# Kernel tuning notes

Hardware: AMD Instinct MI355X
Metric: run time of the kernel (lower is better)

Reference implementation:

```python
import jax, jax.numpy as jnp
from jax import lax
import numpy as np

EPS = 1e-5
DN = ('NCHW', 'OIHW', 'NCHW')


def conv_s2(x, w):
    # Conv2d k=4 s=2 p=1, no bias
    return lax.conv_general_dilated(x, w, (2, 2), [(1, 1), (1, 1)], dimension_numbers=DN)


def deconv_s2(x, w):
    # ConvTranspose2d k=4 s=2 p=1; torch weight layout (in, out, kH, kW)
    w_ = jnp.flip(w, (2, 3)).transpose(1, 0, 2, 3)  # -> (out, in, kH, kW)
    return lax.conv_general_dilated(x, w_, (1, 1), [(2, 2), (2, 2)],
                                    lhs_dilation=(2, 2), dimension_numbers=DN)


def bn_train(x, gamma, beta):
    # BatchNorm2d in training mode: batch stats over (N, H, W), biased variance
    m = jnp.mean(x, axis=(0, 2, 3), keepdims=True)
    v = jnp.var(x, axis=(0, 2, 3), keepdims=True)
    g = gamma.reshape(1, -1, 1, 1)
    b = beta.reshape(1, -1, 1, 1)
    return (x - m) * jax.lax.rsqrt(v + EPS) * g + b


def lrelu(x):
    return jnp.where(x >= 0, x, 0.2 * x)


def setup_inputs() -> dict:
    key = jax.random.key(0)
    ks = jax.random.split(key, 32)
    nef = 64
    d = {}
    d['x'] = jax.random.normal(ks[0], (256, 3, 64, 64), dtype=jnp.float32)
    # encoder conv weights (O, I, 4, 4), init N(0, 0.02)
    d['w1'] = 0.02 * jax.random.normal(ks[1], (nef, 3, 4, 4), jnp.float32)
    d['w2'] = 0.02 * jax.random.normal(ks[2], (nef * 2, nef, 4, 4), jnp.float32)
    d['w3'] = 0.02 * jax.random.normal(ks[3], (nef * 4, nef * 2, 4, 4), jnp.float32)
    d['w4'] = 0.02 * jax.random.normal(ks[4], (nef * 8, nef * 4, 4, 4), jnp.float32)
    # bn params: weight ~ N(1, 0.02), bias = 0
    for i, c in enumerate([nef, nef * 2, nef * 4, nef * 8]):
        d[f'g{i+1}'] = 1.0 + 0.02 * jax.random.normal(ks[5 + i], (c,), jnp.float32)
        d[f'b{i+1}'] = jnp.zeros((c,), jnp.float32)
    # 512 channel-wise Linear(16,16): torch default init U(-1/4, 1/4)
    bound = 1.0 / 4.0
    d['cw_w'] = jax.random.uniform(ks[9], (512, 16, 16), jnp.float32, -bound, bound)
    d['cw_b'] = jax.random.uniform(ks[10], (512, 16), jnp.float32, -bound, bound)
    # decoder deconv weights in torch layout (in, out, 4, 4)
    d['dw1'] = 0.02 * jax.random.normal(ks[11], (nef * 8, nef * 4, 4, 4), jnp.float32)
    d['dw2'] = 0.02 * jax.random.normal(ks[12], (nef * 4, nef * 2, 4, 4), jnp.float32)
    d['dw3'] = 0.02 * jax.random.normal(ks[13], (nef * 2, nef, 4, 4), jnp.float32)
    d['dw4'] = 0.02 * jax.random.normal(ks[14], (nef, 3, 4, 4), jnp.float32)
    for i, c in enumerate([nef * 4, nef * 2, nef]):
        d[f'dg{i+1}'] = 1.0 + 0.02 * jax.random.normal(ks[15 + i], (c,), jnp.float32)
        d[f'db{i+1}'] = jnp.zeros((c,), jnp.float32)
    return d


def reference(x, w1, w2, w3, w4, g1, b1, g2, b2, g3, b3, g4, b4,
              cw_w, cw_b, dw1, dw2, dw3, dw4, dg1, db1, dg2, db2, dg3, db3):
    h = lrelu(bn_train(conv_s2(x, w1), g1, b1))
    h = lrelu(bn_train(conv_s2(h, w2), g2, b2))
    h = lrelu(bn_train(conv_s2(h, w3), g3, b3))
    h = lrelu(bn_train(conv_s2(h, w4), g4, b4))  # (B, 512, 4, 4)
    B, C, H, W = h.shape
    flat = h.reshape(B, C, H * W)  # (B, 512, 16)
    # per-channel Linear: y[b,c,t] = sum_s flat[b,c,s] * cw_w[c,t,s] + cw_b[c,t]
    flat = jnp.einsum('bcs,cts->bct', flat, cw_w) + cw_b[None, :, :]
    h = flat.reshape(B, C, H, W)
    h = jax.nn.relu(bn_train(deconv_s2(h, dw1), dg1, db1))
    h = jax.nn.relu(bn_train(deconv_s2(h, dw2), dg2, db2))
    h = jax.nn.relu(bn_train(deconv_s2(h, dw3), dg3, db3))
    return jnp.tanh(deconv_s2(h, dw4))
```

## Files before the change

kernel.cpp:

```cpp
#include <hip/hip_runtime.h>
#include <math.h>

typedef _Float16 f16;
typedef __attribute__((ext_vector_type(8))) _Float16 f16x8;
typedef __attribute__((ext_vector_type(16))) float f32x16;

union U64x2 { unsigned long long u[2]; f16x8 v; };
union Q16   { uint4 q; unsigned long long u[2]; };

constexpr int ilog2c(int x) { return x <= 1 ? 0 : 1 + ilog2c(x >> 1); }

__device__ __forceinline__ float fast_tanh(float x) {
    float e = __expf(2.f * x);
    return (e - 1.f) / (e + 1.f);
}

__device__ __forceinline__ void barrier_no_vmdrain() {
    asm volatile("s_waitcnt lgkmcnt(0)" ::: "memory");
    __builtin_amdgcn_sched_barrier(0);
    __builtin_amdgcn_s_barrier();
    __builtin_amdgcn_sched_barrier(0);
}

template<int CIN,int IH,int IW,int OH,int OW,int COUT,int COB,int SPT,int KS,
         int CO_FR,bool DEC,bool PAIR>
__global__ __launch_bounds__(256,2) void mfma_conv(
    const f16* __restrict__ xin, const f16* __restrict__ wp,
    f16* __restrict__ out16, float* __restrict__ out32, size_t ps,
    float* __restrict__ psumF, float* __restrict__ psqF)
{
    constexpr int OHo  = DEC ? OH/2 : OH;
    constexpr int OWo  = DEC ? OW/2 : OW;
    constexpr int KTOT = CIN * (DEC ? 4 : 16);
    constexpr int CH   = (KTOT/64) / KS;
    constexpr int RPT  = CIN / 64;
    constexpr int RSH  = (RPT==1?0:RPT==2?1:RPT==4?2:3);
    constexpr int WSTR = CIN * 16;
    constexpr int TPR  = 256 / COB;
    constexpr int SPB  = OHo * OWo;
    constexpr int LSPB = ilog2c(SPB);
    constexpr int LOWo = ilog2c(OWo);

    static_assert(!PAIR || (RPT >= 2 && CH % 2 == 0), "PAIR needs RPT>=2");
    constexpr int CHU  = PAIR ? CH/2 : CH;
    constexpr int RW   = PAIR ? 32 : 16;
    constexpr int PM   = PAIR ? 15 : 7;
    constexpr int KKN  = PAIR ? 8 : 4;
    constexpr int XU4  = PAIR ? 16 : 8;
    constexpr int WSEG = (PAIR ? 128 : 64)/TPR;
    constexpr int WU4  = WSEG / 8;

    __shared__ unsigned long long Xs[SPT*RW];
    __shared__ unsigned long long Wls[COB*RW];

    const int t   = threadIdx.x;
    const int bx  = blockIdx.x;
    const int cob = blockIdx.y;
    const int bz  = blockIdx.z;
    const int par = DEC ? (bz & 3) : 0;
    const int ks  = DEC ? (bz >> 2) : bz;
    const int poh = par >> 1, pw = par & 1;

    const int gsp_s = bx*SPT + t;
    const int img_s = gsp_s >> LSPB;
    const int r_s   = gsp_s & (SPB-1);
    const int oy_s  = r_s >> LOWo;
    const int ox_s  = r_s & (OWo-1);

    const int wco   = t / TPR;
    const int wpart = t % TPR;
    const f16* wbase = wp + (size_t)(cob*COB + wco)*WSTR + wpart*WSEG;

    const int wave = t >> 6, lane = t & 63, half = lane >> 5, l31 = lane & 31;
    const int co_w = (wave >> 1) * (CO_FR*32);
    const int sp_w = (wave & 1) * 128;
    const int swz  = l31 & PM;

    f32x16 acc[CO_FR][4];
    #pragma unroll
    for (int i = 0; i < CO_FR; ++i)
        #pragma unroll
        for (int b = 0; b < 4; ++b)
            #pragma unroll
            for (int r = 0; r < 16; ++r) acc[i][b][r] = 0.f;

    uint4 xreg[XU4];
    uint4 wreg[WU4];

    auto issue = [&](int cc) {
        const int gc  = ks*CH + (PAIR ? 2*cc : cc);
        const int tap = gc >> RSH;
        const int ci0 = (gc & (RPT-1)) << 6;
        int kh, kw, ih, iw;
        if (DEC) {
            const int t2h = tap >> 1, t2w = tap & 1;
            kh = (1-poh) + 2*t2h; kw = (1-pw) + 2*t2w;
            ih = oy_s + poh - t2h; iw = ox_s + pw - t2w;
        } else {
            kh = tap >> 2; kw = tap & 3;
            ih = 2*oy_s - 1 + kh; iw = 2*ox_s - 1 + kw;
        }
        const int woff = (kh*4 + kw)*CIN + ci0;
        const uint4* wsrc = (const uint4*)(wbase + woff);
        #pragma unroll
        for (int j = 0; j < WU4; ++j) wreg[j] = wsrc[j];
        const bool ok = (unsigned)ih < (unsigned)IH && (unsigned)iw < (unsigned)IW;
        if (ok) {
            const uint4* xsrc = (const uint4*)
                (xin + ((size_t)(img_s*IH + ih)*IW + iw)*CIN + ci0);
            #pragma unroll
            for (int j = 0; j < XU4; ++j) xreg[j] = xsrc[j];
        } else {
            #pragma unroll
            for (int j = 0; j < XU4; ++j) xreg[j] = uint4{0u,0u,0u,0u};
        }
    };

    issue(0);

    for (int cc = 0; cc < CHU; ++cc) {
        if (cc) barrier_no_vmdrain();

        #pragma unroll
        for (int j = 0; j < WU4; ++j) {
            Q16 v; v.q = wreg[j];
            const int lp = wpart*WU4 + j;
            const int u0 = wco*RW + ((lp ^ (wco & PM)) << 1);
            Wls[u0]   = v.u[0];
            Wls[u0+1] = v.u[1];
        }
        {
            #pragma unroll
            for (int j = 0; j < XU4; ++j) {
                Q16 v; v.q = xreg[j];
                const int u0 = t*RW + ((j ^ (t & PM)) << 1);
                Xs[u0]   = v.u[0];
                Xs[u0+1] = v.u[1];
            }
        }

        if (cc + 1 < CHU) issue(cc + 1);

        asm volatile("s_waitcnt lgkmcnt(0)" ::: "memory");
        __builtin_amdgcn_sched_barrier(0);
        __builtin_amdgcn_s_barrier();
        __builtin_amdgcn_sched_barrier(0);

        #pragma unroll
        for (int kk = 0; kk < KKN; ++kk) {
            const int so = ((kk*2 + half) ^ swz) << 1;
            f16x8 wf[CO_FR], xf[4];
            #pragma unroll
            for (int i = 0; i < CO_FR; ++i) {
                U64x2 u; const int rw = (co_w + i*32 + l31)*RW + so;
                u.u[0] = Wls[rw]; u.u[1] = Wls[rw+1]; wf[i] = u.v;
            }
            #pragma unroll
            for (int b = 0; b < 4; ++b) {
                U64x2 u; const int rx = (sp_w + b*32 + l31)*RW + so;
                u.u[0] = Xs[rx]; u.u[1] = Xs[rx+1]; xf[b] = u.v;
            }
            #pragma unroll
            for (int i = 0; i < CO_FR; ++i)
                #pragma unroll
                for (int b = 0; b < 4; ++b)
                    acc[i][b] = __builtin_amdgcn_mfma_f32_32x32x16_f16(
                        xf[b], wf[i], acc[i][b], 0, 0, 0);
        }
    }

    #pragma unroll
    for (int b = 0; b < 4; ++b) {
        #pragma unroll
        for (int q = 0; q < 4; ++q) {
            #pragma unroll
            for (int r2 = 0; r2 < 4; ++r2) {
                const int sp_loc = sp_w + b*32 + q*8 + 4*half + r2;
                const int gsp    = bx*SPT + sp_loc;
                size_t base;
                if (DEC) {
                    const int img = gsp >> LSPB;
                    const int r   = gsp & (SPB-1);
                    const int oh  = 2*(r >> LOWo) + poh;
                    const int ow  = 2*(r & (OWo-1)) + pw;
                    base = ((size_t)(img*OH + oh)*OW + ow)*COUT + cob*COB;
                } else {
                    base = (size_t)gsp*COUT + cob*COB;
                }
                #pragma unroll
                for (int i = 0; i < CO_FR; ++i) {
                    const int co_l = co_w + i*32 + l31;
                    const float v  = acc[i][b][q*4 + r2];
                    if (KS == 1) out16[base + co_l] = (_Float16)v;
                    else         out32[(size_t)ks*ps + base + co_l] = v;
                }
            }
        }
    }

    if (KS == 1 && psumF != nullptr) {
        float sArr[CO_FR], qArr[CO_FR];
        #pragma unroll
        for (int i = 0; i < CO_FR; ++i) {
            float s = 0.f, q = 0.f;
            #pragma unroll
            for (int b = 0; b < 4; ++b)
                #pragma unroll
                for (int r = 0; r < 16; ++r) {
                    const float v = acc[i][b][r];
                    s += v; q += v * v;
                }
            s += __shfl_down(s, 32);
            q += __shfl_down(q, 32);
            sArr[i] = s; qArr[i] = q;
        }
        __syncthreads();
        float* LS = (float*)Xs;
        float* LQ = LS + 4*CO_FR*32;
        if (half == 0) {
            #pragma unroll
            for (int i = 0; i < CO_FR; ++i) {
                LS[(wave*CO_FR + i)*32 + l31] = sArr[i];
                LQ[(wave*CO_FR + i)*32 + l31] = qArr[i];
            }
        }
        __syncthreads();
        if (t < COB) {
            constexpr int KSH = (CO_FR == 1 ? 5 : 6);
            const int k  = t >> KSH;
            const int ii = (CO_FR == 1) ? 0 : ((t >> 5) & 1);
            const int l  = t & 31;
            const int i0 = ((2*k)  *CO_FR + ii)*32 + l;
            const int i1 = ((2*k+1)*CO_FR + ii)*32 + l;
            atomicAdd(psumF + cob*COB + t, LS[i0] + LS[i1]);
            atomicAdd(psqF  + cob*COB + t, LQ[i0] + LQ[i1]);
        }
    }
}

__global__ __launch_bounds__(256,2) void conv1_mfma(
    const f16* __restrict__ xp, const f16* __restrict__ wp,
    f16* __restrict__ out, float* __restrict__ psumF, float* __restrict__ psqF)
{
    __shared__ unsigned long long Xs[256*16];
    __shared__ unsigned long long Wls[64*16];
    const int t = threadIdx.x, bx = blockIdx.x;

    {
        const int r = t >> 2, part = t & 3;
        const uint4* src = (const uint4*)(wp + r*64 + part*16);
        Q16 v0; v0.q = src[0];
        Q16 v1; v1.q = src[1];
        const int a0 = r*16 + (((part*2)   ^ (r & 7)) << 1);
        const int a1 = r*16 + (((part*2+1) ^ (r & 7)) << 1);
        Wls[a0]   = v0.u[0]; Wls[a0+1] = v0.u[1];
        Wls[a1]   = v1.u[0]; Wls[a1+1] = v1.u[1];
    }
    {
        const int gsp = bx*256 + t;
        const int n = gsp >> 10, r = gsp & 1023;
        const int oy = r >> 5, ox = r & 31;
        const int ih0 = 2*oy - 1, iw0 = 2*ox - 1;
        #pragma unroll
        for (int tap = 0; tap < 16; ++tap) {
            const int ih = ih0 + (tap >> 2), iw = iw0 + (tap & 3);
            unsigned long long v = 0ull;
            if ((unsigned)ih < 64u && (unsigned)iw < 64u)
                v = *(const unsigned long long*)(xp + (((size_t)n*64 + ih)*64 + iw)*4);
            const int u = t*16 + (((tap >> 1) ^ (t & 7)) << 1) + (tap & 1);
            Xs[u] = v;
        }
    }
    __syncthreads();

    const int wave = t >> 6, lane = t & 63, half = lane >> 5, l31 = lane & 31;
    const int co_w = (wave >> 1) * 32;
    const int sp_w = (wave & 1) * 128;
    const int swz  = l31 & 7;

    f32x16 acc[4];
    #pragma unroll
    for (int b = 0; b < 4; ++b)
        #pragma unroll
        for (int r = 0; r < 16; ++r) acc[b][r] = 0.f;

    #pragma unroll
    for (int kk = 0; kk < 4; ++kk) {
        const int so = ((kk*2 + half) ^ swz) << 1;
        U64x2 uw; const int rw = (co_w + l31)*16 + so;
        uw.u[0] = Wls[rw]; uw.u[1] = Wls[rw+1];
        #pragma unroll
        for (int b = 0; b < 4; ++b) {
            U64x2 ux; const int rx = (sp_w + b*32 + l31)*16 + so;
            ux.u[0] = Xs[rx]; ux.u[1] = Xs[rx+1];
            acc[b] = __builtin_amdgcn_mfma_f32_32x32x16_f16(
                ux.v, uw.v, acc[b], 0, 0, 0);
        }
    }
    #pragma unroll
    for (int b = 0; b < 4; ++b)
        #pragma unroll
        for (int q = 0; q < 4; ++q)
            #pragma unroll
            for (int r2 = 0; r2 < 4; ++r2) {
                const int sp_loc = sp_w + b*32 + q*8 + 4*half + r2;
                out[(size_t)(bx*256 + sp_loc)*64 + co_w + l31] =
                    (_Float16)acc[b][q*4 + r2];
            }

    float s = 0.f, q = 0.f;
    #pragma unroll
    for (int b = 0; b < 4; ++b)
        #pragma unroll
        for (int r = 0; r < 16; ++r) {
            const float v = acc[b][r];
            s += v; q += v * v;
        }
    s += __shfl_down(s, 32);
    q += __shfl_down(q, 32);
    __syncthreads();
    {
        float* LS = (float*)Xs;
        float* LQ = LS + 128;
        if (half == 0) {
            LS[wave*32 + l31] = s;
            LQ[wave*32 + l31] = q;
        }
        __syncthreads();
        if (t < 64) {
            const int k = t >> 5, l = t & 31;
            atomicAdd(psumF + t, LS[(2*k)*32 + l] + LS[(2*k+1)*32 + l]);
            atomicAdd(psqF  + t, LQ[(2*k)*32 + l] + LQ[(2*k+1)*32 + l]);
        }
    }
}

__global__ __launch_bounds__(256,2) void deconv3_pwf(
    const f16* __restrict__ xin, const f16* __restrict__ wp,
    f16* __restrict__ out, float* __restrict__ psumF, float* __restrict__ psqF)
{
    __shared__ unsigned long long Xs[256*16];
    __shared__ unsigned long long Wls[2][64*16];

    const int t   = threadIdx.x;
    const int bx  = blockIdx.x;
    const int poh = blockIdx.y;

    const int gsp_s = bx*256 + t;
    const int img_s = gsp_s >> 8;
    const int r_s   = gsp_s & 255;
    const int oy_s  = r_s >> 4;
    const int ox_s  = r_s & 15;

    const int wco   = t >> 2;
    const int wpart = t & 3;
    const f16* wbase = wp + (size_t)wco*2048 + wpart*16;

    const int wave = t >> 6, lane = t & 63, half = lane >> 5, l31 = lane & 31;
    const int co_w = (wave >> 1) * 32;
    const int sp_w = (wave & 1) * 128;
    const int swz  = l31 & 7;

    f32x16 acc[2][4];
    #pragma unroll
    for (int p = 0; p < 2; ++p)
        #pragma unroll
        for (int b = 0; b < 4; ++b)
            #pragma unroll
            for (int r = 0; r < 16; ++r) acc[p][b][r] = 0.f;

    uint4 xreg[8];
    uint4 wregP[2][2];

    auto issue = [&](int cc) {
        const int seg  = cc & 1;
        const int rest = cc >> 1;
        const int dwi  = rest % 3;
        const int t2h  = rest / 3;
        const int dh = poh - t2h, dw = dwi - 1;
        const int ih = oy_s + dh, iw = ox_s + dw;
        const int ci0 = seg << 6;
        #pragma unroll
        for (int p = 0; p < 2; ++p) {
            const int t2w = p - dw;
            if (t2w == 0 || t2w == 1) {
                const int kh = (1-poh) + 2*t2h, kw = (1-p) + 2*t2w;
                const uint4* wsrc = (const uint4*)(wbase + (kh*4 + kw)*128 + ci0);
                wregP[p][0] = wsrc[0];
                wregP[p][1] = wsrc[1];
            }
        }
        const bool ok = (unsigned)ih < 16u && (unsigned)iw < 16u;
        if (ok) {
            const uint4* xsrc = (const uint4*)
                (xin + ((size_t)(img_s*16 + ih)*16 + iw)*128 + ci0);
            #pragma unroll
            for (int j = 0; j < 8; ++j) xreg[j] = xsrc[j];
        } else {
            #pragma unroll
            for (int j = 0; j < 8; ++j) xreg[j] = uint4{0u,0u,0u,0u};
        }
    };

    issue(0);

    for (int cc = 0; cc < 12; ++cc) {
        const int rest = cc >> 1;
        const int dw   = rest % 3 - 1;

        if (cc) barrier_no_vmdrain();

        #pragma unroll
        for (int p = 0; p < 2; ++p) {
            const int t2w = p - dw;
            if (t2w == 0 || t2w == 1) {
                #pragma unroll
                for (int j = 0; j < 2; ++j) {
                    Q16 v; v.q = wregP[p][j];
                    const int lp = wpart*2 + j;
                    const int u0 = wco*16 + ((lp ^ (wco & 7)) << 1);
                    Wls[p][u0]   = v.u[0];
                    Wls[p][u0+1] = v.u[1];
                }
            }
        }
        #pragma unroll
        for (int j = 0; j < 8; ++j) {
            Q16 v; v.q = xreg[j];
            const int u0 = t*16 + ((j ^ (t & 7)) << 1);
            Xs[u0]   = v.u[0];
            Xs[u0+1] = v.u[1];
        }

        if (cc + 1 < 12) issue(cc + 1);

        asm volatile("s_waitcnt lgkmcnt(0)" ::: "memory");
        __builtin_amdgcn_sched_barrier(0);
        __builtin_amdgcn_s_barrier();
        __builtin_amdgcn_sched_barrier(0);

        #pragma unroll
        for (int kk = 0; kk < 4; ++kk) {
            const int so = ((kk*2 + half) ^ swz) << 1;
            f16x8 xf[4];
            #pragma unroll
            for (int b = 0; b < 4; ++b) {
                U64x2 u; const int rx = (sp_w + b*32 + l31)*16 + so;
                u.u[0] = Xs[rx]; u.u[1] = Xs[rx+1]; xf[b] = u.v;
            }
            #pragma unroll
            for (int p = 0; p < 2; ++p) {
                const int t2w = p - dw;
                if (t2w == 0 || t2w == 1) {
                    U64x2 uw; const int rw = (co_w + l31)*16 + so;
                    uw.u[0] = Wls[p][rw]; uw.u[1] = Wls[p][rw+1];
                    #pragma unroll
                    for (int b = 0; b < 4; ++b)
                        acc[p][b] = __builtin_amdgcn_mfma_f32_32x32x16_f16(
                            xf[b], uw.v, acc[p][b], 0, 0, 0);
                }
            }
        }
    }

    #pragma unroll
    for (int p = 0; p < 2; ++p) {
        #pragma unroll
        for (int b = 0; b < 4; ++b) {
            #pragma unroll
            for (int q = 0; q < 4; ++q) {
                #pragma unroll
                for (int r2 = 0; r2 < 4; ++r2) {
                    const int sp_loc = sp_w + b*32 + q*8 + 4*half + r2;
                    const int gsp    = bx*256 + sp_loc;
                    const int img    = gsp >> 8;
                    const int r      = gsp & 255;
                    const int oh     = 2*(r >> 4) + poh;
                    const int ow     = 2*(r & 15) + p;
                    const size_t base = ((size_t)(img*32 + oh)*32 + ow)*64;
                    out[base + co_w + l31] = (_Float16)acc[p][b][q*4 + r2];
                }
            }
        }
    }

    if (psumF != nullptr) {
        float s = 0.f, q = 0.f;
        #pragma unroll
        for (int p = 0; p < 2; ++p)
            #pragma unroll
            for (int b = 0; b < 4; ++b)
                #pragma unroll
                for (int r = 0; r < 16; ++r) {
                    const float v = acc[p][b][r];
                    s += v; q += v * v;
                }
        s += __shfl_down(s, 32);
        q += __shfl_down(q, 32);
        __syncthreads();
        float* LS = (float*)Xs;
        float* LQ = LS + 128;
        if (half == 0) {
            LS[wave*32 + l31] = s;
            LQ[wave*32 + l31] = q;
        }
        __syncthreads();
        if (t < 64) {
            const int k = t >> 5, l = t & 31;
            atomicAdd(psumF + t, LS[(2*k)*32 + l] + LS[(2*k+1)*32 + l]);
            atomicAdd(psqF  + t, LQ[(2*k)*32 + l] + LQ[(2*k+1)*32 + l]);
        }
    }
}

static constexpr int D4P0[4] = {0,0,1,1};
static constexpr int D4KH0[4]= {3,3,3,3};
static constexpr int D4KW0[4]= {3,1,2,0};
static constexpr int D4DW0[4]= {-1,0,0,1};
static constexpr int D4P1[8] = {0,0,1,1,2,2,3,3};
static constexpr int D4KH1[8]= {1,1,1,1,2,2,2,2};
static constexpr int D4KW1[8]= {3,1,2,0,3,1,2,0};
static constexpr int D4DW1[8]= {-1,0,0,1,-1,0,0,1};
static constexpr int D4P2[4] = {2,2,3,3};
static constexpr int D4KH2[4]= {0,0,0,0};
static constexpr int D4KW2[4]= {3,1,2,0};
static constexpr int D4DW2[4]= {-1,0,0,1};

#define D4_PHASE(DH, PA, KHA, KWA, DWA, NC, LEAD, HASNEXT, NEXTDH)           \
    {                                                                        \
        if (LEAD) barrier_no_vmdrain();                                      \
        uint4 wregc[NC];                                                     \
        _Pragma("unroll")                                                    \
        for (int i = 0; i < NC; ++i)                                         \
            wregc[i] = *(const uint4*)                                       \
                (wp + wco*1024 + (KHA[i]*4 + KWA[i])*64 + wpart*8);          \
        {                                                                    \
            const int c7 = colA & 7;                                         \
            _Pragma("unroll")                                                \
            for (int j = 0; j < 8; ++j) {                                    \
                Q16 v; v.q = xreg[j];                                        \
                const int u0 = t*16 + ((j ^ c7) << 1);                       \
                Xs[u0] = v.u[0]; Xs[u0+1] = v.u[1];                          \
            }                                                                \
        }                                                                    \
        if ((t & 15) == 0) {                                                 \
            const int u2 = 256 + (t >> 4);                                   \
            const int col2 = u2 - 238;               \
            const int iy = R0 + (DH) + 7, ix = col2 - 1;                     \
            const int c7 = col2 & 7;                                         \
            const bool ok = (unsigned)iy < 32u && (unsigned)ix < 32u;        \
            if (ok) {                                                        \
                const uint4* s = (const uint4*)                              \
                    (xin + ((size_t)(img*32 + iy)*32 + ix)*64);              \
                _Pragma("unroll")                                            \
                for (int j = 0; j < 8; ++j) {                                \
                    Q16 v; v.q = s[j];                                       \
                    const int u0 = u2*16 + ((j ^ c7) << 1);                  \
                    Xs[u0] = v.u[0]; Xs[u0+1] = v.u[1];                      \
                }                                                            \
            } else {                                                         \
                _Pragma("unroll")                                            \
                for (int j = 0; j < 8; ++j) {                                \
                    const int u0 = u2*16 + ((j ^ c7) << 1);                  \
                    Xs[u0] = 0ull; Xs[u0+1] = 0ull;                          \
                }                                                            \
            }                                                                \
        }                                                                    \
        _Pragma("unroll")                                                    \
        for (int i = 0; i < NC; ++i) {                                       \
            Q16 v; v.q = wregc[i];                                           \
            const int u0 = wco*16 + ((wpart ^ (wco & 7)) << 1);              \
            Wls[i][u0] = v.u[0]; Wls[i][u0+1] = v.u[1];                      \
        }                                                                    \
        if (HASNEXT) issueX(NEXTDH);                                         \
        asm volatile("s_waitcnt lgkmcnt(0)" ::: "memory");                   \
        __builtin_amdgcn_sched_barrier(0);                                   \
        __builtin_amdgcn_s_barrier();                                        \
        __builtin_amdgcn_sched_barrier(0);                                   \
        _Pragma("unroll")                                                    \
        for (int i = 0; i < NC; ++i) {                                       \
            const int dwv = DWA[i], p = PA[i];                               \
            const int colx = l31 + dwv + 1;                                  \
            const int cx7  = colx & 7;                                       \
            _Pragma("unroll")                                                \
            for (int kk = 0; kk < 4; ++kk) {                                 \
                const int sw = ((kk*2 + half) ^ (l31 & 7)) << 1;             \
                const int sx = ((kk*2 + half) ^ cx7) << 1;                   \
                U64x2 uw; const int rwi = l31*16 + sw;                       \
                uw.u[0] = Wls[i][rwi]; uw.u[1] = Wls[i][rwi+1];              \
                _Pragma("unroll")                                            \
                for (int b = 0; b < 2; ++b) {                                \
                    const int unit = (wave*2 + b)*34 + colx;                 \
                    U64x2 ux; const int rx = unit*16 + sx;                   \
                    ux.u[0] = Xs[rx]; ux.u[1] = Xs[rx+1];                    \
                    acc[p][b] = __builtin_amdgcn_mfma_f32_32x32x16_f16(      \
                        uw.v, ux.v, acc[p][b], 0, 0, 0);                     \
                }                                                            \
            }                                                                \
        }                                                                    \
    }

__global__ __launch_bounds__(256,2) void deconv4_mfma(
    const f16* __restrict__ xin, const f16* __restrict__ wp,
    float* __restrict__ out)
{
    __shared__ unsigned long long Xs[272*16];
    __shared__ unsigned long long Wls[8][32*16];

    const int t   = threadIdx.x;
    const int bx  = blockIdx.x;

    const int img = (bx*256) >> 10;
    const int R0  = ((bx*256) & 1023) >> 5;

    const int wco   = t >> 3;
    const int wpart = t & 7;

    const int wave = t >> 6, lane = t & 63, half = lane >> 5, l31 = lane & 31;
    const int sp_w = wave * 64;

    const int rowA = t / 34, colA = t % 34;

    f32x16 acc[4][2];
    #pragma unroll
    for (int p = 0; p < 4; ++p)
        #pragma unroll
        for (int b = 0; b < 2; ++b)
            #pragma unroll
            for (int r = 0; r < 16; ++r) acc[p][b][r] = 0.f;

    uint4 xreg[8];

    auto issueX = [&](int dh) {
        const int iy = R0 + dh + rowA, ix = colA - 1;
        const bool ok = (unsigned)iy < 32u && (unsigned)ix < 32u;
        if (ok) {
            const uint4* s = (const uint4*)
                (xin + ((size_t)(img*32 + iy)*32 + ix)*64);
            #pragma unroll
            for (int j = 0; j < 8; ++j) xreg[j] = s[j];
        } else {
            #pragma unroll
            for (int j = 0; j < 8; ++j) xreg[j] = uint4{0u,0u,0u,0u};
        }
    };

    issueX(-1);

    D4_PHASE(-1, D4P0, D4KH0, D4KW0, D4DW0, 4, false, true, 0)
    D4_PHASE( 0, D4P1, D4KH1, D4KW1, D4DW1, 8, true,  true, 1)
    D4_PHASE( 1, D4P2, D4KH2, D4KW2, D4DW2, 4, true,  false, 0)

    if (half == 0) {
        #pragma unroll
        for (int p = 0; p < 4; ++p) {
            const int poh = p >> 1, pw = p & 1;
            #pragma unroll
            for (int b = 0; b < 2; ++b) {
                const int gsp = bx*256 + sp_w + b*32 + l31;
                const int im  = gsp >> 10;
                const int r   = gsp & 1023;
                const int oh  = 2*(r >> 5) + poh;
                const int ow  = 2*(r & 31) + pw;
                #pragma unroll
                for (int co = 0; co < 3; ++co)
                    out[(((size_t)im*3 + co)*64 + oh)*64 + ow] =
                        fast_tanh(acc[p][b][co]);
            }
        }
    }
}

__global__ __launch_bounds__(256) void prep_x(
    const float* __restrict__ x, f16* __restrict__ xp)
{
    const int i = blockIdx.x*256 + threadIdx.x;
    const int n = i >> 12, p = i & 4095;
    const float* b = x + (size_t)n*12288 + p;
    union { _Float16 h[4]; unsigned long long u; } o;
    o.h[0] = (_Float16)b[0];
    o.h[1] = (_Float16)b[4096];
    o.h[2] = (_Float16)b[8192];
    o.h[3] = (_Float16)0.f;
    *(unsigned long long*)(xp + (size_t)i*4) = o.u;
}

__global__ __launch_bounds__(256) void prep_w1(
    const float* __restrict__ w1, f16* __restrict__ wp)
{
    const int e = blockIdx.x*256 + threadIdx.x;
    const int co = e >> 6, k = e & 63, tap = k >> 2, ci = k & 3;
    const float v = (ci < 3) ? w1[(co*3 + ci)*16 + tap] : 0.f;
    wp[e] = (_Float16)v;
}

__global__ __launch_bounds__(256) void prep_w4(
    const float* __restrict__ dw4, f16* __restrict__ wp)
{
    const int e = blockIdx.x*256 + threadIdx.x;
    const int co = e >> 10, r = e & 1023, khw = r >> 6, ci = r & 63;
    const float v = (co < 3) ? dw4[(ci*3 + co)*16 + khw] : 0.f;
    wp[e] = (_Float16)v;
}

__global__ __launch_bounds__(256) void prep_w(
    const float* __restrict__ w2, const float* __restrict__ w3,
    const float* __restrict__ w4, const float* __restrict__ dw1,
    const float* __restrict__ dw2, const float* __restrict__ dw3,
    f16* __restrict__ dst)
{
    const int e = blockIdx.x*256 + threadIdx.x;
    float v;
    if (e < 131072) {
        int co = e >> 10, r = e & 1023, khw = r >> 6, ci = r & 63;
        v = w2[(co*64 + ci)*16 + khw];
    } else if (e < 655360) {
        int l = e - 131072;
        int co = l >> 11, r = l & 2047, khw = r >> 7, ci = r & 127;
        v = w3[(co*128 + ci)*16 + khw];
    } else if (e < 2752512) {
        int l = e - 655360;
        int co = l >> 12, r = l & 4095, khw = r >> 8, ci = r & 255;
        v = w4[(co*256 + ci)*16 + khw];
    } else if (e < 4849664) {
        int l = e - 2752512;
        int co = l >> 13, r = l & 8191, khw = r >> 9, ci = r & 511;
        v = dw1[(ci*256 + co)*16 + khw];
    } else if (e < 5373952) {
        int l = e - 4849664;
        int co = l >> 12, r = l & 4095, khw = r >> 8, ci = r & 255;
        v = dw2[(ci*128 + co)*16 + khw];
    } else {
        int l = e - 5373952;
        int co = l >> 11, r = l & 2047, khw = r >> 7, ci = r & 127;
        v = dw3[(ci*64 + co)*16 + khw];
    }
    dst[e] = (_Float16)v;
}

template<typename T, int P>
__global__ __launch_bounds__(256) void bn_partial(
    const T* __restrict__ x, size_t ps, float* __restrict__ psum,
    float* __restrict__ psq, int C, int rowsPerS, int S)
{
    const int s = blockIdx.x;
    const int c = (blockIdx.y << 6) + (threadIdx.x & 63);
    float a = 0.f, q = 0.f;
    const int rEnd = (s + 1) * rowsPerS;
    for (int r = s*rowsPerS + (threadIdx.x >> 6); r < rEnd; r += 4) {
        float v = 0.f;
        #pragma unroll
        for (int p = 0; p < P; ++p)
            v += (float)x[p*ps + (size_t)r * C + c];
        a += v; q += v * v;
    }
    __shared__ float ls[256], lq[256];
    ls[threadIdx.x] = a; lq[threadIdx.x] = q;
    __syncthreads();
    if (threadIdx.x < 64) {
        a = ls[threadIdx.x] + ls[threadIdx.x+64] + ls[threadIdx.x+128] + ls[threadIdx.x+192];
        q = lq[threadIdx.x] + lq[threadIdx.x+64] + lq[threadIdx.x+128] + lq[threadIdx.x+192];
        psum[c * S + s] = a; psq[c * S + s] = q;
    }
}

__global__ __launch_bounds__(256) void bn_finalize(
    const float* __restrict__ psum, const float* __restrict__ psq,
    const float* __restrict__ gamma, const float* __restrict__ beta,
    float* __restrict__ scale, float* __restrict__ shift,
    int C, int S, float inv_count)
{
    int c = blockIdx.x * 256 + threadIdx.x;
    if (c >= C) return;
    float s = 0.f, q = 0.f;
    for (int i = 0; i < S; ++i) { s += psum[c*S + i]; q += psq[c*S + i]; }
    float m   = s * inv_count;
    float var = q * inv_count - m * m;
    var = var < 0.f ? 0.f : var;
    float sc = gamma[c] * rsqrtf(var + 1e-5f);
    scale[c] = sc;
    shift[c] = beta[c] - m * sc;
}

__global__ __launch_bounds__(256) void bn_act16f(
    f16* __restrict__ x, const float* __restrict__ psum, const float* __restrict__ psq,
    const float* __restrict__ gamma, const float* __restrict__ beta,
    int Cmask, float inv_count, float slope, size_t n8)
{
    const size_t base = (size_t)blockIdx.x*256 + threadIdx.x;
    const int c0 = (int)((base * 8) & (size_t)Cmask);
    float sc[8], sh[8];
    #pragma unroll
    for (int j = 0; j < 8; ++j) {
        const int c = c0 + j;
        float m   = psum[c] * inv_count;
        float var = psq[c] * inv_count - m * m;
        var = var < 0.f ? 0.f : var;
        float s = gamma[c] * rsqrtf(var + 1e-5f);
        sc[j] = s;
        sh[j] = beta[c] - m * s;
    }
    const size_t stride = (size_t)gridDim.x * 256;
    for (size_t i = base; i < n8; i += stride) {
        union { uint4 u; _Float16 h[8]; } a;
        a.u = *(const uint4*)(x + i*8);
        #pragma unroll
        for (int j = 0; j < 8; ++j) {
            float v = (float)a.h[j] * sc[j] + sh[j];
            a.h[j] = (_Float16)(v >= 0.f ? v : slope * v);
        }
        *(uint4*)(x + i*8) = a.u;
    }
}

template<int P>
__global__ __launch_bounds__(256) void bn_act32(
    const float* __restrict__ x, size_t ps, f16* __restrict__ y,
    const float* __restrict__ sc, const float* __restrict__ sh,
    int Cmask, float slope)
{
    const size_t i8 = ((size_t)blockIdx.x*256 + threadIdx.x) * 8;
    float xv[8] = {0,0,0,0,0,0,0,0};
    #pragma unroll
    for (int p = 0; p < P; ++p) {
        float4 v0 = *(const float4*)(x + p*ps + i8);
        float4 v1 = *(const float4*)(x + p*ps + i8 + 4);
        xv[0]+=v0.x; xv[1]+=v0.y; xv[2]+=v0.z; xv[3]+=v0.w;
        xv[4]+=v1.x; xv[5]+=v1.y; xv[6]+=v1.z; xv[7]+=v1.w;
    }
    union { uint4 u; _Float16 h[8]; } a;
    const int c0 = (int)(i8 & (size_t)Cmask);
    #pragma unroll
    for (int j = 0; j < 8; ++j) {
        float v = xv[j] * sc[c0+j] + sh[c0+j];
        a.h[j] = (_Float16)(v >= 0.f ? v : slope * v);
    }
    *(uint4*)(y + i8) = a.u;
}

__global__ __launch_bounds__(256) void chanlin16(
    const f16* __restrict__ in, const float* __restrict__ w,
    const float* __restrict__ bias, f16* __restrict__ out)
{
    const int i = blockIdx.x*256 + threadIdx.x;
    const int c  = i & 511;
    const int bt = i >> 9;
    const int b  = bt >> 4, tt = bt & 15;
    const f16* src = in + ((size_t)b*16)*512 + c;
    const float* wr = w + ((size_t)c*16 + tt)*16;
    float acc = bias[c*16 + tt];
    #pragma unroll
    for (int s = 0; s < 16; ++s)
        acc = fmaf((float)src[s*512], wr[s], acc);
    out[i] = (_Float16)acc;
}

extern "C" void kernel_launch(void* const* d_in, const int* in_sizes, int n_in,
                              void* d_out, int out_size, void* d_ws, size_t ws_size,
                              hipStream_t stream)
{
    const float* x   = (const float*)d_in[0];
    const float* w1  = (const float*)d_in[1];
    const float* w2  = (const float*)d_in[2];
    const float* w3  = (const float*)d_in[3];
    const float* w4  = (const float*)d_in[4];
    const float* g1  = (const float*)d_in[5];
    const float* b1  = (const float*)d_in[6];
    const float* g2  = (const float*)d_in[7];
    const float* b2  = (const float*)d_in[8];
    const float* g3  = (const float*)d_in[9];
    const float* b3  = (const float*)d_in[10];
    const float* g4  = (const float*)d_in[11];
    const float* b4  = (const float*)d_in[12];
    const float* cww = (const float*)d_in[13];
    const float* cwb = (const float*)d_in[14];
    const float* dw1 = (const float*)d_in[15];
    const float* dw2 = (const float*)d_in[16];
    const float* dw3 = (const float*)d_in[17];
    const float* dw4 = (const float*)d_in[18];
    const float* dg1 = (const float*)d_in[19];
    const float* db1 = (const float*)d_in[20];
    const float* dg2 = (const float*)d_in[21];
    const float* db2 = (const float*)d_in[22];
    const float* dg3 = (const float*)d_in[23];
    const float* db3 = (const float*)d_in[24];

    char* WS = (char*)d_ws;
    float* psum  = (float*)WS;
    float* psq   = (float*)(WS + 65536);
    float* scale = (float*)(WS + 131072);
    float* shift = (float*)(WS + 133120);
    float* fst   = (float*)(WS + 196608);
    f16* slotA   = (f16*)(WS + 262144);
    f16* slotB   = (f16*)(WS + 262144 + 33554432);
    f16* wprep   = (f16*)(WS + 84148224);
    f16* wprep1  = wprep + 5505024;
    f16* wprep4  = wprep1 + 4096;

    f16*   A_hi  = slotA + 8388608;
    float* pB    = (float*)slotB;
    f16*   xpack = slotA;

    float* fs0 = fst;          float* fs1 = fst + 1024;
    float* fs2 = fst + 2048;   float* fs4 = fst + 4096;
    float* fs5 = fst + 5120;   float* fs6 = fst + 6144;

    hipMemsetAsync(fst, 0, 28672, stream);
    prep_w<<<21504, 256, 0, stream>>>(w2, w3, w4, dw1, dw2, dw3, wprep);
    prep_w1<<<16, 256, 0, stream>>>(w1, wprep1);
    prep_w4<<<128, 256, 0, stream>>>(dw4, wprep4);
    prep_x<<<4096, 256, 0, stream>>>(x, xpack);

    conv1_mfma<<<1024, 256, 0, stream>>>(xpack, wprep1, slotB, fs0, fs0 + 512);
    bn_act16f<<<2048, 256, 0, stream>>>(slotB, fs0, fs0 + 512, g1, b1, 63,
                                        1.f/262144.f, 0.2f, (size_t)2097152);

    mfma_conv<64,32,32,16,16,128, 128,256,1,2,false,false><<<dim3(256,1,1), 256, 0, stream>>>(
        slotB, wprep, slotA, nullptr, 0, fs1, fs1 + 512);
    bn_act16f<<<2048, 256, 0, stream>>>(slotA, fs1, fs1 + 512, g2, b2, 127,
                                        1.f/65536.f, 0.2f, (size_t)1048576);

    mfma_conv<128,16,16,8,8,256, 64,256,1,1,false,false><<<dim3(64,4,1), 256, 0, stream>>>(
        slotA, wprep + 131072, A_hi, nullptr, 0, fs2, fs2 + 512);
    bn_act16f<<<2048, 256, 0, stream>>>(A_hi, fs2, fs2 + 512, g3, b3, 255,
                                        1.f/16384.f, 0.2f, (size_t)524288);

    mfma_conv<256,8,8,4,4,512, 128,256,4,2,false,false><<<dim3(16,4,4), 256, 0, stream>>>(
        A_hi, wprep + 655360, nullptr, pB, (size_t)2097152, nullptr, nullptr);
    bn_partial<float,4><<<dim3(32,8), 256, 0, stream>>>(pB, (size_t)2097152, psum, psq, 512, 128, 32);
    bn_finalize<<<2, 256, 0, stream>>>(psum, psq, g4, b4, scale, shift, 512, 32, 1.f/4096.f);
    bn_act32<4><<<1024, 256, 0, stream>>>(pB, (size_t)2097152, slotA, scale, shift, 511, 0.2f);

    chanlin16<<<8192, 256, 0, stream>>>(slotA, cww, cwb, slotB);

    mfma_conv<512,4,4,8,8,256, 64,256,1,1,true,false><<<dim3(16,4,4), 256, 0, stream>>>(
        slotB, wprep + 2752512, A_hi, nullptr, 0, fs4, fs4 + 512);
    bn_act16f<<<2048, 256, 0, stream>>>(A_hi, fs4, fs4 + 512, dg1, db1, 255,
                                        1.f/16384.f, 0.f, (size_t)524288);

    mfma_conv<256,8,8,16,16,128, 128,256,1,2,true,false><<<dim3(64,1,4), 256, 0, stream>>>(
        A_hi, wprep + 4849664, slotB, nullptr, 0, fs5, fs5 + 512);
    bn_act16f<<<2048, 256, 0, stream>>>(slotB, fs5, fs5 + 512, dg2, db2, 127,
                                        1.f/65536.f, 0.f, (size_t)1048576);

    deconv3_pwf<<<dim3(256,2), 256, 0, stream>>>(
        slotB, wprep + 5373952, slotA, fs6, fs6 + 512);
    bn_act16f<<<2048, 256, 0, stream>>>(slotA, fs6, fs6 + 512, dg3, db3, 63,
                                        1.f/262144.f, 0.f, (size_t)2097152);

    deconv4_mfma<<<1024, 256, 0, stream>>>(slotA, wprep4, (float*)d_out);
}
```

Baseline: 520.5 us.

## Stage halo-padded input tile once per row phase and reuse across column taps

The deconv3 kernel now processes one image per block and loads a 16x18 column-halo-padded input tile into shared memory. MFMA reads then index shifted columns for each of the four (p, dw) taps, instead of reloading the input from global memory for every dw offset. This cuts the main loop from 12 chunks to 4 phases and reduces global input traffic. The cost is more shared memory for the tile and four weight slices, an extra partial load for halo rows, and more irregular swizzled LDS addressing.

```diff
diff --git a/kernel.cpp b/kernel.cpp
--- a/kernel.cpp
+++ b/kernel.cpp
@@ -335,22 +335,25 @@
     }
 }
 
+static constexpr int D3P[4]  = {0, 0, 1, 1};
+static constexpr int D3DW[4] = {0,-1, 1, 0};
+static constexpr int D3KW[4] = {1, 3, 0, 2};
+
 __global__ __launch_bounds__(256,2) void deconv3_pwf(
     const f16* __restrict__ xin, const f16* __restrict__ wp,
     f16* __restrict__ out, float* __restrict__ psumF, float* __restrict__ psqF)
 {
-    __shared__ unsigned long long Xs[256*16];
-    __shared__ unsigned long long Wls[2][64*16];
+    __shared__ unsigned long long Xs[288*16];
+    __shared__ unsigned long long Wls[4][64*16];
 
     const int t   = threadIdx.x;
-    const int bx  = blockIdx.x;
+    const int img = blockIdx.x;
     const int poh = blockIdx.y;
 
-    const int gsp_s = bx*256 + t;
-    const int img_s = gsp_s >> 8;
-    const int r_s   = gsp_s & 255;
-    const int oy_s  = r_s >> 4;
-    const int ox_s  = r_s & 15;
+    const int rowA = t / 18, colA = t % 18;
+    const int u2   = 256 + (t >> 1);
+    const int row2 = u2 / 18, col2 = u2 % 18;
+    const int jh   = (t & 1) * 4;
 
     const int wco   = t >> 2;
     const int wpart = t & 3;
@@ -370,69 +373,92 @@
             for (int r = 0; r < 16; ++r) acc[p][b][r] = 0.f;
 
     uint4 xreg[8];
-    uint4 wregP[2][2];
-
-    auto issue = [&](int cc) {
-        const int seg  = cc & 1;
-        const int rest = cc >> 1;
-        const int dwi  = rest % 3;
-        const int t2h  = rest / 3;
-        const int dh = poh - t2h, dw = dwi - 1;
-        const int ih = oy_s + dh, iw = ox_s + dw;
+    uint4 xregT[4];
+
+    auto issueX = [&](int ph) {
+        const int seg = ph >> 1;
+        const int dh  = poh - (ph & 1);
         const int ci0 = seg << 6;
-        #pragma unroll
-        for (int p = 0; p < 2; ++p) {
-            const int t2w = p - dw;
-            if (t2w == 0 || t2w == 1) {
-                const int kh = (1-poh) + 2*t2h, kw = (1-p) + 2*t2w;
-                const uint4* wsrc = (const uint4*)(wbase + (kh*4 + kw)*128 + ci0);
-                wregP[p][0] = wsrc[0];
-                wregP[p][1] = wsrc[1];
-            }
-        }
-        const bool ok = (unsigned)ih < 16u && (unsigned)iw < 16u;
-        if (ok) {
-            const uint4* xsrc = (const uint4*)
-                (xin + ((size_t)(img_s*16 + ih)*16 + iw)*128 + ci0);
-            #pragma unroll
-            for (int j = 0; j < 8; ++j) xreg[j] = xsrc[j];
-        } else {
-            #pragma unroll
-            for (int j = 0; j < 8; ++j) xreg[j] = uint4{0u,0u,0u,0u};
+        {
+            const int iy = rowA + dh, ix = colA - 1;
+            const bool ok = (unsigned)iy < 16u && (unsigned)ix < 16u;
+            if (ok) {
+                const uint4* s = (const uint4*)
+                    (xin + ((size_t)(img*16 + iy)*16 + ix)*128 + ci0);
+                #pragma unroll
+                for (int j = 0; j < 8; ++j) xreg[j] = s[j];
+            } else {
+                #pragma unroll
+                for (int j = 0; j < 8; ++j) xreg[j] = uint4{0u,0u,0u,0u};
+            }
+        }
+        if (t < 64) {
+            const int iy = row2 + dh, ix = col2 - 1;
+            const bool ok = (unsigned)iy < 16u && (unsigned)ix < 16u;
+            if (ok) {
+                const uint4* s = (const uint4*)
+                    (xin + ((size_t)(img*16 + iy)*16 + ix)*128 + ci0 + jh*8);
+                #pragma unroll
+                for (int j = 0; j < 4; ++j) xregT[j] = s[j];
+            } else {
+                #pragma unroll
+                for (int j = 0; j < 4; ++j) xregT[j] = uint4{0u,0u,0u,0u};
+            }
         }
     };
 
-    issue(0);
-
-    for (int cc = 0; cc < 12; ++cc) {
-        const int rest = cc >> 1;
-        const int dw   = rest % 3 - 1;
-
-        if (cc) barrier_no_vmdrain();
-
-        #pragma unroll
-        for (int p = 0; p < 2; ++p) {
-            const int t2w = p - dw;
-            if (t2w == 0 || t2w == 1) {
-                #pragma unroll
-                for (int j = 0; j < 2; ++j) {
-                    Q16 v; v.q = wregP[p][j];
-                    const int lp = wpart*2 + j;
-                    const int u0 = wco*16 + ((lp ^ (wco & 7)) << 1);
-                    Wls[p][u0]   = v.u[0];
-                    Wls[p][u0+1] = v.u[1];
-                }
-            }
-        }
-        #pragma unroll
-        for (int j = 0; j < 8; ++j) {
-            Q16 v; v.q = xreg[j];
-            const int u0 = t*16 + ((j ^ (t & 7)) << 1);
-            Xs[u0]   = v.u[0];
-            Xs[u0+1] = v.u[1];
-        }
-
-        if (cc + 1 < 12) issue(cc + 1);
+    issueX(0);
+
+    for (int ph = 0; ph < 4; ++ph) {
+        const int seg = ph >> 1;
+        const int t2h = ph & 1;
+        const int kh  = (1 - poh) + 2*t2h;
+        const int ci0 = seg << 6;
+
+        if (ph) barrier_no_vmdrain();
+
+        uint4 wregc[4][2];
+        #pragma unroll
+        for (int i = 0; i < 4; ++i) {
+            const uint4* ws = (const uint4*)(wbase + (kh*4 + D3KW[i])*128 + ci0);
+            wregc[i][0] = ws[0];
+            wregc[i][1] = ws[1];
+        }
+
+        {
+            const int c7 = colA & 7;
+            #pragma unroll
+            for (int j = 0; j < 8; ++j) {
+                Q16 v; v.q = xreg[j];
+                const int u0 = t*16 + ((j ^ c7) << 1);
+                Xs[u0]   = v.u[0];
+                Xs[u0+1] = v.u[1];
+            }
+        }
+        if (t < 64) {
+            const int c72 = col2 & 7;
+            #pragma unroll
+            for (int j = 0; j < 4; ++j) {
+                Q16 v; v.q = xregT[j];
+                const int sj = jh + j;
+                const int u0 = u2*16 + ((sj ^ c72) << 1);
+                Xs[u0]   = v.u[0];
+                Xs[u0+1] = v.u[1];
+            }
+        }
+        #pragma unroll
+        for (int i = 0; i < 4; ++i) {
+            #pragma unroll
+            for (int j = 0; j < 2; ++j) {
+                Q16 v; v.q = wregc[i][j];
+                const int lp = wpart*2 + j;
+                const int u0 = wco*16 + ((lp ^ (wco & 7)) << 1);
+                Wls[i][u0]   = v.u[0];
+                Wls[i][u0+1] = v.u[1];
+            }
+        }
+
+        if (ph + 1 < 4) issueX(ph + 1);
 
         asm volatile("s_waitcnt lgkmcnt(0)" ::: "memory");
         __builtin_amdgcn_sched_barrier(0);
@@ -440,24 +466,25 @@
         __builtin_amdgcn_sched_barrier(0);
 
         #pragma unroll
-        for (int kk = 0; kk < 4; ++kk) {
-            const int so = ((kk*2 + half) ^ swz) << 1;
-            f16x8 xf[4];
-            #pragma unroll
-            for (int b = 0; b < 4; ++b) {
-                U64x2 u; const int rx = (sp_w + b*32 + l31)*16 + so;
-                u.u[0] = Xs[rx]; u.u[1] = Xs[rx+1]; xf[b] = u.v;
-            }
-            #pragma unroll
-            for (int p = 0; p < 2; ++p) {
-                const int t2w = p - dw;
-                if (t2w == 0 || t2w == 1) {
-                    U64x2 uw; const int rw = (co_w + l31)*16 + so;
-                    uw.u[0] = Wls[p][rw]; uw.u[1] = Wls[p][rw+1];
-                    #pragma unroll
-                    for (int b = 0; b < 4; ++b)
-                        acc[p][b] = __builtin_amdgcn_mfma_f32_32x32x16_f16(
-                            xf[b], uw.v, acc[p][b], 0, 0, 0);
+        for (int i = 0; i < 4; ++i) {
+            const int p  = D3P[i];
+            const int dw = D3DW[i];
+            #pragma unroll
+            for (int kk = 0; kk < 4; ++kk) {
+                const int sW = ((kk*2 + half) ^ swz) << 1;
+                U64x2 uw; const int rw = (co_w + l31)*16 + sW;
+                uw.u[0] = Wls[i][rw]; uw.u[1] = Wls[i][rw+1];
+                #pragma unroll
+                for (int b = 0; b < 4; ++b) {
+                    const int sp   = sp_w + b*32 + l31;
+                    const int row  = sp >> 4;
+                    const int colx = (sp & 15) + dw + 1;
+                    const int unit = row*18 + colx;
+                    const int sX   = ((kk*2 + half) ^ (colx & 7)) << 1;
+                    U64x2 ux; const int rx = unit*16 + sX;
+                    ux.u[0] = Xs[rx]; ux.u[1] = Xs[rx+1];
+                    acc[p][b] = __builtin_amdgcn_mfma_f32_32x32x16_f16(
+                        ux.v, uw.v, acc[p][b], 0, 0, 0);
                 }
             }
         }
@@ -472,11 +499,8 @@
                 #pragma unroll
                 for (int r2 = 0; r2 < 4; ++r2) {
                     const int sp_loc = sp_w + b*32 + q*8 + 4*half + r2;
-                    const int gsp    = bx*256 + sp_loc;
-                    const int img    = gsp >> 8;
-                    const int r      = gsp & 255;
-                    const int oh     = 2*(r >> 4) + poh;
-                    const int ow     = 2*(r & 15) + p;
+                    const int oh     = 2*(sp_loc >> 4) + poh;
+                    const int ow     = 2*(sp_loc & 15) + p;
                     const size_t base = ((size_t)(img*32 + oh)*32 + ow)*64;
                     out[base + co_w + l31] = (_Float16)acc[p][b][q*4 + r2];
                 }
```

Result: slower. 534.9 us (+2.8%).
